# Optimization experiments

Hardware: AMD Instinct MI355X
Metric: run time of the kernel (lower is better)

The kernel has to match this reference:

```python
import jax, jax.numpy as jnp
import numpy as np

N_NODES = 50000
N_EDGES = 600000
N_GRAPHS = 500


def gcn_conv(x, src, dst, W, b, n_nodes):
    # PyG GCNConv: add self-loops, symmetric normalization D^-1/2 (A+I) D^-1/2, then XW + b
    h = x @ W  # [N, F_out]
    loop = jnp.arange(n_nodes)
    s = jnp.concatenate([src, loop])
    d = jnp.concatenate([dst, loop])
    deg = jax.ops.segment_sum(jnp.ones_like(d, dtype=h.dtype), d, num_segments=n_nodes)
    dinv = jnp.where(deg > 0, jax.lax.rsqrt(jnp.maximum(deg, 1.0)), 0.0)
    norm = dinv[s] * dinv[d]  # [E+N]
    msg = h[s] * norm[:, None]  # gather + scale
    out = jax.ops.segment_sum(msg, d, num_segments=n_nodes)  # scatter-add
    return out + b


def setup_inputs() -> dict:
    key = jax.random.key(0)
    ks = jax.random.split(key, 12)
    F_in, H, Hf, D_out = 128, 128, 64, 1
    x = jax.random.normal(ks[0], (N_NODES, F_in), dtype=jnp.float32)
    edge_index = jax.random.randint(ks[1], (2, N_EDGES), 0, N_NODES, dtype=jnp.int64)
    batch = jnp.sort(jax.random.randint(ks[2], (N_NODES,), 0, N_GRAPHS, dtype=jnp.int64))
    def glorot(k, shape):
        lim = np.sqrt(6.0 / (shape[0] + shape[1]))
        return jax.random.uniform(k, shape, jnp.float32, -lim, lim)
    return {
        "x": x, "edge_index": edge_index, "batch": batch,
        "W1": glorot(ks[3], (F_in, H)), "b1": jnp.zeros((H,), jnp.float32),
        "W2": glorot(ks[4], (H, H)), "b2": jnp.zeros((H,), jnp.float32),
        "W3": glorot(ks[5], (H, H)), "b3": jnp.zeros((H,), jnp.float32),
        "Wf1": glorot(ks[6], (H, Hf)), "bf1": jnp.zeros((Hf,), jnp.float32),
        "Wf2": glorot(ks[7], (Hf, D_out)), "bf2": jnp.zeros((D_out,), jnp.float32),
    }


def reference(x, edge_index, batch, W1, b1, W2, b2, W3, b3, Wf1, bf1, Wf2, bf2):
    src, dst = edge_index[0], edge_index[1]
    n = x.shape[0]
    h = jax.nn.relu(gcn_conv(x, src, dst, W1, b1, n))
    h = jax.nn.relu(gcn_conv(h, src, dst, W2, b2, n))
    h = jax.nn.relu(gcn_conv(h, src, dst, W3, b3, n))
    # global_mean_pool: segment mean over graphs
    sums = jax.ops.segment_sum(h, batch, num_segments=N_GRAPHS)
    cnts = jax.ops.segment_sum(jnp.ones((n,), h.dtype), batch, num_segments=N_GRAPHS)
    hg = sums / jnp.maximum(cnts, 1.0)[:, None]  # [G, 128]
    h = jax.nn.relu(hg @ Wf1 + bf1)
    return h @ Wf2 + bf2
```

## Files before the change

kernel.cpp:

```cpp
#include <hip/hip_runtime.h>

#define N_NODES 50000
#define N_EDGES 600000
#define N_GRAPHS 500
#define F 128

typedef short bf16x8 __attribute__((ext_vector_type(8)));
typedef float f32x4 __attribute__((ext_vector_type(4)));
union U4H8 { uint4 u; bf16x8 h; };

__device__ inline unsigned pk_bf16(float a, float b) {
    unsigned ua = __float_as_uint(a), ub = __float_as_uint(b);
    ua = (ua + 0x7fffu + ((ua >> 16) & 1u)) >> 16;
    ub = (ub + 0x7fffu + ((ub >> 16) & 1u)) >> 16;
    return ua | (ub << 16);
}
__device__ inline float bf16_rnd(float x) {
    unsigned u = __float_as_uint(x);
    u = (u + 0x7fffu + ((u >> 16) & 1u)) & 0xffff0000u;
    return __uint_as_float(u);
}
__device__ inline unsigned short bf16_1(float a) {
    unsigned ua = __float_as_uint(a);
    return (unsigned short)((ua + 0x7fffu + ((ua >> 16) & 1u)) >> 16);
}
#define BF_LO(u) __uint_as_float((u) << 16)
#define BF_HI(u) __uint_as_float((u) & 0xffff0000u)

#define G_CVT  3125
#define G_HIST 2344
#define G_PREPW 24
#define G_BND  196

__global__ __launch_bounds__(256) void k_prep(const float* __restrict__ x, unsigned short* __restrict__ xb,
                                              const int* __restrict__ dst, int* __restrict__ cnt,
                                              const float* __restrict__ W1, const float* __restrict__ W2,
                                              const float* __restrict__ W3,
                                              uint4* __restrict__ Whi, uint4* __restrict__ Wlo,
                                              const int* __restrict__ batch, int* __restrict__ gs) {
    int b = blockIdx.x, tid = threadIdx.x;
    if (b < G_CVT) {
        int idx = b * 256 + tid;
        if (idx < N_NODES * F / 8) {
            const float4* xr = (const float4*)(x + (size_t)idx * 8);
            float4 a = xr[0], c = xr[1];
            uint4 o;
            o.x = pk_bf16(a.x, a.y); o.y = pk_bf16(a.z, a.w);
            o.z = pk_bf16(c.x, c.y); o.w = pk_bf16(c.z, c.w);
            ((uint4*)xb)[idx] = o;
        }
    } else if (b < G_CVT + G_HIST) {
        int e = (b - G_CVT) * 256 + tid;
        if (e < N_EDGES) atomicAdd(&cnt[dst[e]], 1);
    } else if (b < G_CVT + G_HIST + G_PREPW) {
        int idx = (b - G_CVT - G_HIST) * 256 + tid;
        int layer = idx >> 11;
        const float* W = (layer == 0) ? W1 : (layer == 1) ? W2 : W3;
        int t = idx & 2047;
        int lane = t & 63, sc = t >> 6;
        int s = sc >> 3, c = sc & 7;
        int q = lane >> 4, m = lane & 15;
        int k0 = 32 * s + 8 * q, n0 = 16 * c + m;
        float w[8], h[8];
        #pragma unroll
        for (int j = 0; j < 8; ++j) {
            w[j] = W[(k0 + j) * F + n0];
            h[j] = bf16_rnd(w[j]);
        }
        uint4 uh, ul;
        uh.x = pk_bf16(h[0], h[1]); uh.y = pk_bf16(h[2], h[3]);
        uh.z = pk_bf16(h[4], h[5]); uh.w = pk_bf16(h[6], h[7]);
        ul.x = pk_bf16(w[0] - h[0], w[1] - h[1]); ul.y = pk_bf16(w[2] - h[2], w[3] - h[3]);
        ul.z = pk_bf16(w[4] - h[4], w[5] - h[5]); ul.w = pk_bf16(w[6] - h[6], w[7] - h[7]);
        Whi[idx] = uh;
        Wlo[idx] = ul;
    } else {
        int i = (b - G_CVT - G_HIST - G_PREPW) * 256 + tid;
        if (i < N_NODES) {
            int bi = batch[i];
            if (i == 0) {
                for (int g = 0; g <= bi; ++g) gs[g] = 0;
            } else {
                int bp = batch[i - 1];
                for (int g = bp + 1; g <= bi; ++g) gs[g] = i;
            }
            if (i == N_NODES - 1) {
                for (int g = bi + 1; g <= N_GRAPHS; ++g) gs[g] = N_NODES;
            }
        }
    }
}

__global__ __launch_bounds__(256) void k_scan1(const int* __restrict__ cnt, int* __restrict__ row_ptr,
                                               int* __restrict__ blksums, float* __restrict__ dinv,
                                               int* __restrict__ dh, int n) {
    __shared__ int s[256];
    __shared__ int dhl[64];
    int tid = threadIdx.x;
    int i = blockIdx.x * 256 + tid;
    if (tid < 64) dhl[tid] = 0;
    int v = (i < n) ? cnt[i] : 0;
    if (i < n) dinv[i] = rsqrtf((float)(v + 1));
    s[tid] = v;
    __syncthreads();
    if (i < n) atomicAdd(&dhl[v < 63 ? v : 63], 1);
    for (int off = 1; off < 256; off <<= 1) {
        int t = (tid >= off) ? s[tid - off] : 0;
        __syncthreads();
        s[tid] += t;
        __syncthreads();
    }
    if (i < n) row_ptr[i] = s[tid] - v;
    if (tid == 255) blksums[blockIdx.x] = s[255];
    __syncthreads();
    if (tid < 64 && dhl[tid] > 0) atomicAdd(&dh[tid], dhl[tid]);
}

__global__ __launch_bounds__(256) void k_scan23(int* __restrict__ row_ptr, const int* __restrict__ blksums,
                                                const int* __restrict__ dh, int* __restrict__ dhoff,
                                                int* __restrict__ dcur, int n, int ne) {
    __shared__ int s[256];
    int tid = threadIdx.x;
    s[tid] = (tid < (int)blockIdx.x) ? blksums[tid] : 0;
    __syncthreads();
    for (int off = 128; off > 0; off >>= 1) {
        if (tid < off) s[tid] += s[tid + off];
        __syncthreads();
    }
    int base = s[0];
    int i = blockIdx.x * 256 + tid;
    if (i < n) row_ptr[i] += base;
    if (i == 0) row_ptr[n] = ne;
    if (blockIdx.x == 0 && tid < 64) {
        int v = dh[tid];
        int x = v;
        #pragma unroll
        for (int off = 1; off < 64; off <<= 1) {
            int t = __shfl_up(x, off, 64);
            if (tid >= off) x += t;
        }
        dhoff[tid] = x - v;
        dcur[tid] = 0;
    }
}

#define G_FILL 2344
#define G_PLACE 196
__global__ __launch_bounds__(256) void k_fill(const int* __restrict__ src, const int* __restrict__ dst,
                                              const int* __restrict__ row_ptr, int* __restrict__ cnt,
                                              const float* __restrict__ dinv,
                                              int2* __restrict__ esw,
                                              const int* __restrict__ dhoff, int* __restrict__ dcur,
                                              int* __restrict__ perm, int ne) {
    __shared__ int lh[64];
    __shared__ int lbase[64];
    int b = blockIdx.x, tid = threadIdx.x;
    if (b < G_FILL) {
        int e = b * 256 + tid;
        if (e < ne) {
            int d = dst[e];
            int s = src[e];
            int pos = row_ptr[d] + atomicSub(&cnt[d], 1) - 1;
            esw[pos] = make_int2(s, __float_as_int(dinv[s]));
        }
    } else {
        int i = (b - G_FILL) * 256 + tid;
        if (tid < 64) lh[tid] = 0;
        __syncthreads();
        int deg = 0, rank = 0;
        bool valid = (i < N_NODES);
        if (valid) {
            deg = row_ptr[i + 1] - row_ptr[i];
            if (deg > 63) deg = 63;
            rank = atomicAdd(&lh[deg], 1);
        }
        __syncthreads();
        if (tid < 64 && lh[tid] > 0)
            lbase[tid] = atomicAdd(&dcur[tid], lh[tid]);
        __syncthreads();
        if (valid) perm[dhoff[deg] + lbase[deg] + rank] = i;
    }
}

#define TN 32
#define GP2 136
#define CAPG 32
__global__ __launch_bounds__(256) void k_fused(const int* __restrict__ row_ptr,
                                               const int2* __restrict__ esw,
                                               const float* __restrict__ dinv,
                                               const int* __restrict__ perm,
                                               const unsigned short* __restrict__ Hin,
                                               const uint4* __restrict__ Whi,
                                               const uint4* __restrict__ Wlo,
                                               const float* __restrict__ bias,
                                               unsigned short* __restrict__ Hout, int n) {
    __shared__ unsigned short Gb[TN * GP2];
    __shared__ uint2 eLg[TN][CAPG];
    __shared__ int nodeL[TN], begL[TN], endL[TN];
    __shared__ float ddl[TN];
    int tid = threadIdx.x;
    int d0 = blockIdx.x * TN;
    int grp = tid >> 4, sub = tid & 15;

    if (tid < TN) {
        int slot = d0 + tid;
        int node = (slot < n) ? perm[slot] : -1;
        nodeL[tid] = node;
        if (node >= 0) {
            begL[tid] = row_ptr[node];
            endL[tid] = row_ptr[node + 1];
            ddl[tid] = dinv[node];
        } else {
            begL[tid] = 0; endL[tid] = 0; ddl[tid] = 0.f;
        }
    }
    __syncthreads();

    #pragma unroll 1
    for (int n2 = 0; n2 < 2; ++n2) {
        int gi = grp + 16 * n2;
        int node = nodeL[gi];
        int beg = begL[gi], end = endL[gi];
        int deg = end - beg;
        float dd = ddl[gi];

        int degc = deg < CAPG ? deg : CAPG;
        for (int i = sub; i < degc; i += 16) eLg[gi][i] = ((const uint2*)esw)[beg + i];

        float4 accL = make_float4(0.f, 0.f, 0.f, 0.f);
        float4 accH = make_float4(0.f, 0.f, 0.f, 0.f);
        if (node >= 0) {
            uint4 srow = ((const uint4*)(Hin + (size_t)node * F))[sub];
            float ws = dd * dd;
            accL.x = BF_LO(srow.x) * ws;
            accL.y = BF_HI(srow.x) * ws;
            accL.z = BF_LO(srow.y) * ws;
            accL.w = BF_HI(srow.y) * ws;
            accH.x = BF_LO(srow.z) * ws;
            accH.y = BF_HI(srow.z) * ws;
            accH.z = BF_LO(srow.w) * ws;
            accH.w = BF_HI(srow.w) * ws;
            for (int c = 0; c < deg; c += 8) {
                int sjs[8];
                #pragma unroll
                for (int j = 0; j < 8; ++j) {
                    int e = c + j;
                    int sj = node;
                    if (e < deg) sj = (e < CAPG) ? (int)eLg[gi][e].x
                                                 : ((const uint2*)esw)[beg + e].x;
                    sjs[j] = sj;
                }
                uint4 rows[8];
                #pragma unroll
                for (int j = 0; j < 8; ++j)
                    rows[j] = ((const uint4*)(Hin + (size_t)sjs[j] * F))[sub];
                #pragma unroll
                for (int j = 0; j < 8; ++j) {
                    int e = c + j;
                    float wj = 0.f;
                    if (e < deg) {
                        unsigned wb = (e < CAPG) ? eLg[gi][e].y
                                                 : (unsigned)((const uint2*)esw)[beg + e].y;
                        wj = __uint_as_float(wb) * dd;
                    }
                    accL.x = fmaf(BF_LO(rows[j].x), wj, accL.x);
                    accL.y = fmaf(BF_HI(rows[j].x), wj, accL.y);
                    accL.z = fmaf(BF_LO(rows[j].y), wj, accL.z);
                    accL.w = fmaf(BF_HI(rows[j].y), wj, accL.w);
                    accH.x = fmaf(BF_LO(rows[j].z), wj, accH.x);
                    accH.y = fmaf(BF_HI(rows[j].z), wj, accH.y);
                    accH.z = fmaf(BF_LO(rows[j].w), wj, accH.z);
                    accH.w = fmaf(BF_HI(rows[j].w), wj, accH.w);
                }
            }
        }
        {
            uint4 o;
            o.x = pk_bf16(accL.x, accL.y);
            o.y = pk_bf16(accL.z, accL.w);
            o.z = pk_bf16(accH.x, accH.y);
            o.w = pk_bf16(accH.z, accH.w);
            *(uint4*)&Gb[gi * GP2 + 8 * sub] = o;
        }
    }
    __syncthreads();

    int wave = tid >> 6, lane = tid & 63;
    int q = lane >> 4, m = lane & 15;
    f32x4 acc0[2], acc1[2];
    acc0[0] = (f32x4){0.f, 0.f, 0.f, 0.f};
    acc0[1] = (f32x4){0.f, 0.f, 0.f, 0.f};
    acc1[0] = (f32x4){0.f, 0.f, 0.f, 0.f};
    acc1[1] = (f32x4){0.f, 0.f, 0.f, 0.f};
    #pragma unroll
    for (int s = 0; s < 4; ++s) {
        U4H8 a0, a1;
        a0.u = *(const uint4*)&Gb[m * GP2 + 32 * s + 8 * q];
        a1.u = *(const uint4*)&Gb[(m + 16) * GP2 + 32 * s + 8 * q];
        #pragma unroll
        for (int cc = 0; cc < 2; ++cc) {
            int c = wave * 2 + cc;
            U4H8 bh, bl;
            bh.u = Whi[(s * 8 + c) * 64 + lane];
            bl.u = Wlo[(s * 8 + c) * 64 + lane];
            acc0[cc] = __builtin_amdgcn_mfma_f32_16x16x32_bf16(a0.h, bh.h, acc0[cc], 0, 0, 0);
            acc0[cc] = __builtin_amdgcn_mfma_f32_16x16x32_bf16(a0.h, bl.h, acc0[cc], 0, 0, 0);
            acc1[cc] = __builtin_amdgcn_mfma_f32_16x16x32_bf16(a1.h, bh.h, acc1[cc], 0, 0, 0);
            acc1[cc] = __builtin_amdgcn_mfma_f32_16x16x32_bf16(a1.h, bl.h, acc1[cc], 0, 0, 0);
        }
    }
    __syncthreads();

    #pragma unroll
    for (int cc = 0; cc < 2; ++cc) {
        int c = wave * 2 + cc;
        float bb = bias[16 * c + m];
        #pragma unroll
        for (int r = 0; r < 4; ++r) {
            Gb[(4 * q + r) * GP2 + 16 * c + m] = bf16_1(fmaxf(acc0[cc][r] + bb, 0.f));
            Gb[(16 + 4 * q + r) * GP2 + 16 * c + m] = bf16_1(fmaxf(acc1[cc][r] + bb, 0.f));
        }
    }
    __syncthreads();
    {
        int row = tid >> 4, c8 = tid & 15;
        #pragma unroll
        for (int rr = 0; rr < 2; ++rr) {
            int r2 = row + 16 * rr;
            int onode = nodeL[r2];
            if (onode >= 0) {
                uint4 o = *(const uint4*)&Gb[r2 * GP2 + c8 * 8];
                ((uint4*)(Hout + (size_t)onode * F))[c8] = o;
            }
        }
    }
}

__global__ __launch_bounds__(256) void k_pool_fc(const unsigned short* __restrict__ Hb,
                                                 const int* __restrict__ gs,
                                                 const float* __restrict__ Wf1,
                                                 const float* __restrict__ bf1,
                                                 const float* __restrict__ Wf2,
                                                 const float* __restrict__ bf2,
                                                 float* __restrict__ out) {
    int g = blockIdx.x;
    int tid = threadIdx.x;
    int start = gs[g], end = gs[g + 1];

    __shared__ float hs[4][F];
    __shared__ float hg[F];
    int wv = tid >> 6, lane = tid & 63;
    int half = lane >> 5, sub = lane & 31;
    float4 a = make_float4(0.f, 0.f, 0.f, 0.f);
    for (int i = start + wv * 2 + half; i < end; i += 8) {
        uint2 v = ((const uint2*)(Hb + (size_t)i * F))[sub];
        a.x += BF_LO(v.x); a.y += BF_HI(v.x);
        a.z += BF_LO(v.y); a.w += BF_HI(v.y);
    }
    a.x += __shfl_xor(a.x, 32, 64);
    a.y += __shfl_xor(a.y, 32, 64);
    a.z += __shfl_xor(a.z, 32, 64);
    a.w += __shfl_xor(a.w, 32, 64);
    if (half == 0) ((float4*)hs[wv])[sub] = a;
    __syncthreads();
    if (tid < F) {
        float inv = 1.0f / (float)((end - start) > 0 ? (end - start) : 1);
        hg[tid] = (hs[0][tid] + hs[1][tid] + hs[2][tid] + hs[3][tid]) * inv;
    }
    __syncthreads();
    if (tid < 64) {
        float acc = bf1[tid];
        #pragma unroll 4
        for (int f = 0; f < F; ++f) acc = fmaf(hg[f], Wf1[f * 64 + tid], acc);
        float v = fmaxf(acc, 0.f) * Wf2[tid];
        #pragma unroll
        for (int off = 32; off > 0; off >>= 1) v += __shfl_down(v, off, 64);
        if (tid == 0) out[g] = v + bf2[0];
    }
}

extern "C" void kernel_launch(void* const* d_in, const int* in_sizes, int n_in,
                              void* d_out, int out_size, void* d_ws, size_t ws_size,
                              hipStream_t stream) {
    const float* x    = (const float*)d_in[0];
    const int* eidx   = (const int*)d_in[1];
    const int* batch  = (const int*)d_in[2];
    const float* W1   = (const float*)d_in[3];
    const float* b1   = (const float*)d_in[4];
    const float* W2   = (const float*)d_in[5];
    const float* b2   = (const float*)d_in[6];
    const float* W3   = (const float*)d_in[7];
    const float* b3   = (const float*)d_in[8];
    const float* Wf1  = (const float*)d_in[9];
    const float* bf1  = (const float*)d_in[10];
    const float* Wf2  = (const float*)d_in[11];
    const float* bf2  = (const float*)d_in[12];
    float* out = (float*)d_out;

    const int* src = eidx;
    const int* dst = eidx + N_EDGES;

    char* p = (char*)d_ws;
    unsigned short* Xb  = (unsigned short*)p;  p += (size_t)N_NODES * F * 2;
    unsigned short* H1  = (unsigned short*)p;  p += (size_t)N_NODES * F * 2;
    unsigned short* H2  = (unsigned short*)p;  p += (size_t)N_NODES * F * 2;
    unsigned short* H3  = (unsigned short*)p;  p += (size_t)N_NODES * F * 2;
    int2* esw   = (int2*)p;    p += (size_t)N_EDGES * sizeof(int2);
    uint4* Whi  = (uint4*)p;   p += (size_t)3 * 2048 * sizeof(uint4);
    uint4* Wlo  = (uint4*)p;   p += (size_t)3 * 2048 * sizeof(uint4);
    float* dinv = (float*)p;   p += (size_t)N_NODES * sizeof(float);
    int* cnt     = (int*)p;    p += (size_t)N_NODES * sizeof(int);
    int* dh      = (int*)p;    p += 64 * sizeof(int);
    int* row_ptr = (int*)p;    p += (size_t)(N_NODES + 1) * sizeof(int);
    int* blksums = (int*)p;    p += 256 * sizeof(int);
    int* gs      = (int*)p;    p += (size_t)(N_GRAPHS + 1) * sizeof(int);
    int* dhoff   = (int*)p;    p += 64 * sizeof(int);
    int* dcur    = (int*)p;    p += 64 * sizeof(int);
    int* perm    = (int*)p;    p += (size_t)N_NODES * sizeof(int);

    dim3 b256(256);
    int gNodes = (N_NODES + 255) / 256;
    int gFused = (N_NODES + TN - 1) / TN;

    hipMemsetAsync(cnt, 0, ((size_t)N_NODES + 64) * sizeof(int), stream);
    k_prep<<<G_CVT + G_HIST + G_PREPW + G_BND, b256, 0, stream>>>(x, Xb, dst, cnt, W1, W2, W3,
                                                                  Whi, Wlo, batch, gs);

    k_scan1<<<gNodes, b256, 0, stream>>>(cnt, row_ptr, blksums, dinv, dh, N_NODES);
    k_scan23<<<gNodes, b256, 0, stream>>>(row_ptr, blksums, dh, dhoff, dcur, N_NODES, N_EDGES);
    k_fill<<<G_FILL + G_PLACE, b256, 0, stream>>>(src, dst, row_ptr, cnt, dinv, esw,
                                                  dhoff, dcur, perm, N_EDGES);

    k_fused<<<gFused, b256, 0, stream>>>(row_ptr, esw, dinv, perm, Xb, Whi,        Wlo,        b1, H1, N_NODES);
    k_fused<<<gFused, b256, 0, stream>>>(row_ptr, esw, dinv, perm, H1, Whi + 2048, Wlo + 2048, b2, H2, N_NODES);
    k_fused<<<gFused, b256, 0, stream>>>(row_ptr, esw, dinv, perm, H2, Whi + 4096, Wlo + 4096, b3, H3, N_NODES);

    k_pool_fc<<<N_GRAPHS, b256, 0, stream>>>(H3, gs, Wf1, bf1, Wf2, bf2, out);
}
```

Baseline: 255.4 us.

## Record edge rank during histogram and store CSR as source-only indices

```diff
diff --git a/kernel.cpp b/kernel.cpp
--- a/kernel.cpp
+++ b/kernel.cpp
@@ -34,6 +34,7 @@
 
 __global__ __launch_bounds__(256) void k_prep(const float* __restrict__ x, unsigned short* __restrict__ xb,
                                               const int* __restrict__ dst, int* __restrict__ cnt,
+                                              int* __restrict__ rnk,
                                               const float* __restrict__ W1, const float* __restrict__ W2,
                                               const float* __restrict__ W3,
                                               uint4* __restrict__ Whi, uint4* __restrict__ Wlo,
@@ -51,7 +52,7 @@
         }
     } else if (b < G_CVT + G_HIST) {
         int e = (b - G_CVT) * 256 + tid;
-        if (e < N_EDGES) atomicAdd(&cnt[dst[e]], 1);
+        if (e < N_EDGES) rnk[e] = atomicAdd(&cnt[dst[e]], 1);
     } else if (b < G_CVT + G_HIST + G_PREPW) {
         int idx = (b - G_CVT - G_HIST) * 256 + tid;
         int layer = idx >> 11;
@@ -147,9 +148,8 @@
 #define G_FILL 2344
 #define G_PLACE 196
 __global__ __launch_bounds__(256) void k_fill(const int* __restrict__ src, const int* __restrict__ dst,
-                                              const int* __restrict__ row_ptr, int* __restrict__ cnt,
-                                              const float* __restrict__ dinv,
-                                              int2* __restrict__ esw,
+                                              const int* __restrict__ row_ptr, const int* __restrict__ rnk,
+                                              int* __restrict__ esrc,
                                               const int* __restrict__ dhoff, int* __restrict__ dcur,
                                               int* __restrict__ perm, int ne) {
     __shared__ int lh[64];
@@ -159,9 +159,7 @@
         int e = b * 256 + tid;
         if (e < ne) {
             int d = dst[e];
-            int s = src[e];
-            int pos = row_ptr[d] + atomicSub(&cnt[d], 1) - 1;
-            esw[pos] = make_int2(s, __float_as_int(dinv[s]));
+            esrc[row_ptr[d] + rnk[e]] = src[e];
         }
     } else {
         int i = (b - G_FILL) * 256 + tid;
@@ -186,7 +184,7 @@
 #define GP2 136
 #define CAPG 32
 __global__ __launch_bounds__(256) void k_fused(const int* __restrict__ row_ptr,
-                                               const int2* __restrict__ esw,
+                                               const int* __restrict__ esrc,
                                                const float* __restrict__ dinv,
                                                const int* __restrict__ perm,
                                                const unsigned short* __restrict__ Hin,
@@ -225,7 +223,10 @@
         float dd = ddl[gi];
 
         int degc = deg < CAPG ? deg : CAPG;
-        for (int i = sub; i < degc; i += 16) eLg[gi][i] = ((const uint2*)esw)[beg + i];
+        for (int i = sub; i < degc; i += 16) {
+            int s = esrc[beg + i];
+            eLg[gi][i] = make_uint2((unsigned)s, (unsigned)__float_as_int(dinv[s]));
+        }
 
         float4 accL = make_float4(0.f, 0.f, 0.f, 0.f);
         float4 accH = make_float4(0.f, 0.f, 0.f, 0.f);
@@ -247,7 +248,7 @@
                     int e = c + j;
                     int sj = node;
                     if (e < deg) sj = (e < CAPG) ? (int)eLg[gi][e].x
-                                                 : ((const uint2*)esw)[beg + e].x;
+                                                 : esrc[beg + e];
                     sjs[j] = sj;
                 }
                 uint4 rows[8];
@@ -259,9 +260,9 @@
                     int e = c + j;
                     float wj = 0.f;
                     if (e < deg) {
-                        unsigned wb = (e < CAPG) ? eLg[gi][e].y
-                                                 : (unsigned)((const uint2*)esw)[beg + e].y;
-                        wj = __uint_as_float(wb) * dd;
+                        float dv = (e < CAPG) ? __uint_as_float(eLg[gi][e].y)
+                                              : dinv[sjs[j]];
+                        wj = dv * dd;
                     }
                     accL.x = fmaf(BF_LO(rows[j].x), wj, accL.x);
                     accL.y = fmaf(BF_HI(rows[j].x), wj, accL.y);
@@ -405,7 +406,8 @@
     unsigned short* H1  = (unsigned short*)p;  p += (size_t)N_NODES * F * 2;
     unsigned short* H2  = (unsigned short*)p;  p += (size_t)N_NODES * F * 2;
     unsigned short* H3  = (unsigned short*)p;  p += (size_t)N_NODES * F * 2;
-    int2* esw   = (int2*)p;    p += (size_t)N_EDGES * sizeof(int2);
+    int* esrc   = (int*)p;     p += (size_t)N_EDGES * sizeof(int);
+    int* rnk    = (int*)p;     p += (size_t)N_EDGES * sizeof(int);
     uint4* Whi  = (uint4*)p;   p += (size_t)3 * 2048 * sizeof(uint4);
     uint4* Wlo  = (uint4*)p;   p += (size_t)3 * 2048 * sizeof(uint4);
     float* dinv = (float*)p;   p += (size_t)N_NODES * sizeof(float);
@@ -423,17 +425,17 @@
     int gFused = (N_NODES + TN - 1) / TN;
 
     hipMemsetAsync(cnt, 0, ((size_t)N_NODES + 64) * sizeof(int), stream);
-    k_prep<<<G_CVT + G_HIST + G_PREPW + G_BND, b256, 0, stream>>>(x, Xb, dst, cnt, W1, W2, W3,
+    k_prep<<<G_CVT + G_HIST + G_PREPW + G_BND, b256, 0, stream>>>(x, Xb, dst, cnt, rnk, W1, W2, W3,
                                                                   Whi, Wlo, batch, gs);
 
     k_scan1<<<gNodes, b256, 0, stream>>>(cnt, row_ptr, blksums, dinv, dh, N_NODES);
     k_scan23<<<gNodes, b256, 0, stream>>>(row_ptr, blksums, dh, dhoff, dcur, N_NODES, N_EDGES);
-    k_fill<<<G_FILL + G_PLACE, b256, 0, stream>>>(src, dst, row_ptr, cnt, dinv, esw,
+    k_fill<<<G_FILL + G_PLACE, b256, 0, stream>>>(src, dst, row_ptr, rnk, esrc,
                                                   dhoff, dcur, perm, N_EDGES);
 
-    k_fused<<<gFused, b256, 0, stream>>>(row_ptr, esw, dinv, perm, Xb, Whi,        Wlo,        b1, H1, N_NODES);
-    k_fused<<<gFused, b256, 0, stream>>>(row_ptr, esw, dinv, perm, H1, Whi + 2048, Wlo + 2048, b2, H2, N_NODES);
-    k_fused<<<gFused, b256, 0, stream>>>(row_ptr, esw, dinv, perm, H2, Whi + 4096, Wlo + 4096, b3, H3, N_NODES);
+    k_fused<<<gFused, b256, 0, stream>>>(row_ptr, esrc, dinv, perm, Xb, Whi,        Wlo,        b1, H1, N_NODES);
+    k_fused<<<gFused, b256, 0, stream>>>(row_ptr, esrc, dinv, perm, H1, Whi + 2048, Wlo + 2048, b2, H2, N_NODES);
+    k_fused<<<gFused, b256, 0, stream>>>(row_ptr, esrc, dinv, perm, H2, Whi + 4096, Wlo + 4096, b3, H3, N_NODES);
 
     k_pool_fc<<<N_GRAPHS, b256, 0, stream>>>(H3, gs, Wf1, bf1, Wf2, bf2, out);
 }
```

Result: faster. 241.7 us (-5.4%).
